# Kernel optimization log

Hardware: AMD Instinct MI355X
Metric: run time of the kernel (lower is better)

Reference implementation:

```python
import jax, jax.numpy as jnp
import numpy as np

N_NODES = 50000
N_EDGES = 800000
NEG_SLOPE = 0.2  # DGL GATConv leaky_relu default


def setup_inputs() -> dict:
    key = jax.random.key(0)
    ks = jax.random.split(key, 10)
    in_feats, n_hidden, n_classes = 256, 64, 47
    h1 = 4  # heads layer 1
    x = jax.random.normal(ks[0], (N_NODES, in_feats), dtype=jnp.float32)
    W1 = jax.random.normal(ks[1], (in_feats, h1 * n_hidden), dtype=jnp.float32) / np.sqrt(in_feats)
    al1 = jax.random.normal(ks[2], (h1, n_hidden), dtype=jnp.float32) * 0.1
    ar1 = jax.random.normal(ks[3], (h1, n_hidden), dtype=jnp.float32) * 0.1
    b1 = jnp.zeros((h1 * n_hidden,), dtype=jnp.float32)
    W2 = jax.random.normal(ks[4], (h1 * n_hidden, n_classes), dtype=jnp.float32) / np.sqrt(h1 * n_hidden)
    al2 = jax.random.normal(ks[5], (1, n_classes), dtype=jnp.float32) * 0.1
    ar2 = jax.random.normal(ks[6], (1, n_classes), dtype=jnp.float32) * 0.1
    b2 = jnp.zeros((n_classes,), dtype=jnp.float32)
    src = jax.random.randint(ks[7], (N_EDGES,), 0, N_NODES, dtype=jnp.int32)
    dst = jnp.sort(jax.random.randint(ks[8], (N_EDGES,), 0, N_NODES, dtype=jnp.int32))
    return {"x": x, "W1": W1, "al1": al1, "ar1": ar1, "b1": b1,
            "W2": W2, "al2": al2, "ar2": ar2, "b2": b2,
            "src": src, "dst": dst}


def gat_conv(h, W, al, ar, b, src, dst, heads, out_dim):
    # Linear projection -> [N, H, D]
    fs = (h @ W).reshape(-1, heads, out_dim)
    # Per-node attention logits: el/er [N, H]
    el = jnp.einsum('nhd,hd->nh', fs, al)
    er = jnp.einsum('nhd,hd->nh', fs, ar)
    # Edge-level attention: e [E, H]
    e = el[src] + er[dst]
    e = jnp.where(e > 0, e, NEG_SLOPE * e)  # leaky_relu
    # Segment softmax over incoming edges of each dst node
    m = jax.lax.stop_gradient(jax.ops.segment_max(e, dst, num_segments=N_NODES))
    ex = jnp.exp(e - m[dst])
    denom = jax.ops.segment_sum(ex, dst, num_segments=N_NODES)
    alpha = ex / denom[dst]  # [E, H]
    # Weighted scatter-aggregate of source features
    msg = alpha[:, :, None] * fs[src]  # [E, H, D]
    out = jax.ops.segment_sum(msg, dst, num_segments=N_NODES)  # [N, H, D]
    return out + b.reshape(1, heads, out_dim)


def reference(x, W1, al1, ar1, b1, W2, al2, ar2, b2, src, dst):
    # Layer 1: GATConv(256 -> 64, 4 heads) + relu activation, flatten heads
    h = gat_conv(x, W1, al1, ar1, b1, src, dst, heads=4, out_dim=64)
    h = jax.nn.relu(h).reshape(N_NODES, -1)  # [N, 256]
    # Layer 2: GATConv(256 -> 47, 1 head), no activation, mean over heads
    h = gat_conv(h, W2, al2, ar2, b2, src, dst, heads=1, out_dim=47)
    return h.mean(axis=1)  # [N, 47]
```

## Files before the change

### kernel.cpp

```cpp
#include <hip/hip_runtime.h>
#include <math.h>

#define NNODES 50000
#define NEDGES 800000
#define NEG_SLOPE 0.2f
#define MPAD 50048
#define CAPW 64

typedef __attribute__((ext_vector_type(8))) short short8;
typedef __attribute__((ext_vector_type(4))) float floatx4;

__device__ __forceinline__ unsigned short f2bf(float f) {
    union { float f; unsigned int u; } v; v.f = f;
    unsigned int r = v.u + 0x7FFFu + ((v.u >> 16) & 1u);
    return (unsigned short)(r >> 16);
}
__device__ __forceinline__ float bf2f(unsigned int s) {
    union { unsigned int u; float f; } v; v.u = s << 16; return v.f;
}
__device__ __forceinline__ float lrelu(float e) { return e > 0.f ? e : NEG_SLOPE * e; }

__global__ __launch_bounds__(256) void prep(const float* __restrict__ x,
                                            const float* __restrict__ W1,
                                            const float* __restrict__ W2,
                                            const int* __restrict__ dst,
                                            unsigned short* __restrict__ xb,
                                            unsigned short* __restrict__ bfrag1,
                                            unsigned short* __restrict__ bfrag2,
                                            unsigned short* __restrict__ h1b,
                                            int* __restrict__ row_ptr) {
    int b = blockIdx.x;
    if (b < 12512) {
        long e = ((long)b * 256 + threadIdx.x) * 4;
        const long NE = (long)NNODES * 256;
        ushort4 o;
        o.x = (e + 0 < NE) ? f2bf(x[e + 0]) : 0;
        o.y = (e + 1 < NE) ? f2bf(x[e + 1]) : 0;
        o.z = (e + 2 < NE) ? f2bf(x[e + 2]) : 0;
        o.w = (e + 3 < NE) ? f2bf(x[e + 3]) : 0;
        *(ushort4*)(xb + e) = o;
    } else if (b < 12708) {
        int n = (b - 12512) * 256 + threadIdx.x;
        if (n > NNODES) return;
        int lo = 0, hi = NEDGES;
        while (lo < hi) {
            int mid = (lo + hi) >> 1;
            if (dst[mid] < n) lo = mid + 1; else hi = mid;
        }
        row_ptr[n] = lo;
    } else if (b < 12740) {
        int c = (b - 12708) * 256 + threadIdx.x;
        int l = c & 63, kk = (c >> 6) & 7, t = c >> 9;
        int n = t * 16 + (l & 15);
        int kbase = kk * 32 + (l >> 4) * 8;
#pragma unroll
        for (int j = 0; j < 8; j++)
            bfrag1[c * 8 + j] = f2bf(W1[(kbase + j) * 256 + n]);
    } else if (b < 12746) {
        int c = (b - 12740) * 256 + threadIdx.x;
        int l = c & 63, kk = (c >> 6) & 7, t = c >> 9;
        int n = t * 16 + (l & 15);
        int kbase = kk * 32 + (l >> 4) * 8;
#pragma unroll
        for (int j = 0; j < 8; j++)
            bfrag2[c * 8 + j] = (n < 47) ? f2bf(W2[(kbase + j) * 47 + n]) : 0;
    } else {
        int row = NNODES + (b - 12746);
        h1b[(size_t)row * 256 + threadIdx.x] = 0;
    }
}

__global__ __launch_bounds__(256) void mfma_gemm1(const unsigned short* __restrict__ xb,
                                                  const unsigned short* __restrict__ bfrag,
                                                  const float* __restrict__ al1,
                                                  const float* __restrict__ ar1,
                                                  unsigned short* __restrict__ fs1b,
                                                  float* __restrict__ el,
                                                  float* __restrict__ er) {
    const int w = threadIdx.x >> 6;
    const int l = threadIdx.x & 63;
    const int bm = blockIdx.x * 128;
    const int head = blockIdx.y;
    const int n0 = head * 64;
    const int lm = l & 15, lk = l >> 4;

    floatx4 acc[2][4];
#pragma unroll
    for (int i = 0; i < 2; i++)
#pragma unroll
        for (int j = 0; j < 4; j++) acc[i][j] = (floatx4){0.f, 0.f, 0.f, 0.f};

    const int t0 = n0 >> 4;
#pragma unroll
    for (int kk = 0; kk < 8; kk++) {
        const unsigned short* abase = xb + (size_t)(bm + w * 32 + lm) * 256 + kk * 32 + lk * 8;
        short8 a0 = *(const short8*)(abase);
        short8 a1 = *(const short8*)(abase + 16 * 256);
        const unsigned short* bbase = bfrag + ((t0 * 8 + kk) * 64 + l) * 8;
        short8 b[4];
#pragma unroll
        for (int j = 0; j < 4; j++) b[j] = *(const short8*)(bbase + j * 8 * 64 * 8);
#pragma unroll
        for (int j = 0; j < 4; j++) {
            acc[0][j] = __builtin_amdgcn_mfma_f32_16x16x32_bf16(a0, b[j], acc[0][j], 0, 0, 0);
            acc[1][j] = __builtin_amdgcn_mfma_f32_16x16x32_bf16(a1, b[j], acc[1][j], 0, 0, 0);
        }
    }
#pragma unroll
    for (int i = 0; i < 2; i++) {
        int row0 = bm + w * 32 + i * 16 + lk * 4;
#pragma unroll
        for (int r = 0; r < 4; r++) {
            int row = row0 + r;
            if (row >= NNODES) continue;
#pragma unroll
            for (int j = 0; j < 4; j++) {
                int col = n0 + j * 16 + lm;
                fs1b[(size_t)row * 256 + col] = f2bf(acc[i][j][r]);
            }
        }
    }
    float alv[4], arv[4];
#pragma unroll
    for (int j = 0; j < 4; j++) {
        alv[j] = al1[head * 64 + j * 16 + lm];
        arv[j] = ar1[head * 64 + j * 16 + lm];
    }
#pragma unroll
    for (int i = 0; i < 2; i++) {
#pragma unroll
        for (int r = 0; r < 4; r++) {
            float pe = 0.f, pr = 0.f;
#pragma unroll
            for (int j = 0; j < 4; j++) {
                float fr = bf2f(f2bf(acc[i][j][r]));
                pe += fr * alv[j];
                pr += fr * arv[j];
            }
#pragma unroll
            for (int off = 1; off < 16; off <<= 1) {
                pe += __shfl_xor(pe, off);
                pr += __shfl_xor(pr, off);
            }
            int row = bm + w * 32 + i * 16 + lk * 4 + r;
            if (lm == 0 && row < NNODES) {
                el[row * 4 + head] = pe;
                er[row * 4 + head] = pr;
            }
        }
    }
}

__global__ __launch_bounds__(256) void mfma_gemm2(const unsigned short* __restrict__ h1b,
                                                  const unsigned short* __restrict__ bfrag,
                                                  const float* __restrict__ al2,
                                                  const float* __restrict__ ar2,
                                                  unsigned short* __restrict__ fs2b,
                                                  float* __restrict__ el,
                                                  float* __restrict__ er) {
    const int w = threadIdx.x >> 6;
    const int l = threadIdx.x & 63;
    const int bm = blockIdx.x * 128;
    const int lm = l & 15, lk = l >> 4;

    floatx4 acc[2][3];
#pragma unroll
    for (int i = 0; i < 2; i++)
#pragma unroll
        for (int j = 0; j < 3; j++) acc[i][j] = (floatx4){0.f, 0.f, 0.f, 0.f};

#pragma unroll
    for (int kk = 0; kk < 8; kk++) {
        const unsigned short* abase = h1b + (size_t)(bm + w * 32 + lm) * 256 + kk * 32 + lk * 8;
        short8 a0 = *(const short8*)(abase);
        short8 a1 = *(const short8*)(abase + 16 * 256);
        const unsigned short* bbase = bfrag + (size_t)(kk * 64 + l) * 8;
        short8 b[3];
#pragma unroll
        for (int j = 0; j < 3; j++) b[j] = *(const short8*)(bbase + j * (8 * 64 * 8));
#pragma unroll
        for (int j = 0; j < 3; j++) {
            acc[0][j] = __builtin_amdgcn_mfma_f32_16x16x32_bf16(a0, b[j], acc[0][j], 0, 0, 0);
            acc[1][j] = __builtin_amdgcn_mfma_f32_16x16x32_bf16(a1, b[j], acc[1][j], 0, 0, 0);
        }
    }
#pragma unroll
    for (int i = 0; i < 2; i++) {
        int row0 = bm + w * 32 + i * 16 + lk * 4;
#pragma unroll
        for (int r = 0; r < 4; r++) {
            int row = row0 + r;
            if (row >= NNODES) continue;
#pragma unroll
            for (int j = 0; j < 3; j++) {
                int col = j * 16 + lm;
                fs2b[(size_t)row * 48 + col] = f2bf(acc[i][j][r]);
            }
        }
    }
    float alv[3], arv[3];
#pragma unroll
    for (int j = 0; j < 3; j++) {
        int col = j * 16 + lm;
        alv[j] = (col < 47) ? al2[col] : 0.f;
        arv[j] = (col < 47) ? ar2[col] : 0.f;
    }
#pragma unroll
    for (int i = 0; i < 2; i++) {
#pragma unroll
        for (int r = 0; r < 4; r++) {
            float pe = 0.f, pr = 0.f;
#pragma unroll
            for (int j = 0; j < 3; j++) {
                float fr = bf2f(f2bf(acc[i][j][r]));
                pe += fr * alv[j];
                pr += fr * arv[j];
            }
#pragma unroll
            for (int off = 1; off < 16; off <<= 1) {
                pe += __shfl_xor(pe, off);
                pr += __shfl_xor(pr, off);
            }
            int row = bm + w * 32 + i * 16 + lk * 4 + r;
            if (lm == 0 && row < NNODES) {
                el[row] = pe;
                er[row] = pr;
            }
        }
    }
}

#define EDGE_ACC(G0, G1, W)                                              \
    a[0]  += (W) * bf2f((G0).x & 0xFFFFu); a[1]  += (W) * bf2f((G0).x >> 16); \
    a[2]  += (W) * bf2f((G0).y & 0xFFFFu); a[3]  += (W) * bf2f((G0).y >> 16); \
    a[4]  += (W) * bf2f((G0).z & 0xFFFFu); a[5]  += (W) * bf2f((G0).z >> 16); \
    a[6]  += (W) * bf2f((G0).w & 0xFFFFu); a[7]  += (W) * bf2f((G0).w >> 16); \
    a[8]  += (W) * bf2f((G1).x & 0xFFFFu); a[9]  += (W) * bf2f((G1).x >> 16); \
    a[10] += (W) * bf2f((G1).y & 0xFFFFu); a[11] += (W) * bf2f((G1).y >> 16); \
    a[12] += (W) * bf2f((G1).z & 0xFFFFu); a[13] += (W) * bf2f((G1).z >> 16); \
    a[14] += (W) * bf2f((G1).w & 0xFFFFu); a[15] += (W) * bf2f((G1).w >> 16);

__global__ __launch_bounds__(256) void agg1(const int* __restrict__ row_ptr,
                                            const int* __restrict__ src,
                                            const float* __restrict__ el,
                                            const float* __restrict__ er,
                                            const unsigned short* __restrict__ fs1b,
                                            const float* __restrict__ b1,
                                            unsigned short* __restrict__ h1b) {
    __shared__ float wcache[4][CAPW * 4];
    __shared__ int   scache[4][CAPW];
    const int q = threadIdx.x >> 6;
    const int l = threadIdx.x & 63;
    const int n = blockIdx.x * 4 + q;
    const int start = row_ptr[n], end = row_ptr[n + 1];
    const int deg = end - start;

    const float4 erv = *(const float4*)(er + n * 4);
    const int g = l >> 4;
    const int c16 = l & 15;
    const int hl = c16 >> 2;
    float a[16] = {};

    if (deg <= CAPW) {
        const bool act = l < deg;
        int sv = 0;
        float e0 = -1e30f, e1 = -1e30f, e2 = -1e30f, e3 = -1e30f;
        if (act) {
            sv = src[start + l];
            float4 e4 = *(const float4*)(el + sv * 4);
            e0 = lrelu(e4.x + erv.x);
            e1 = lrelu(e4.y + erv.y);
            e2 = lrelu(e4.z + erv.z);
            e3 = lrelu(e4.w + erv.w);
        }
        float M0 = e0, M1 = e1, M2 = e2, M3 = e3;
#pragma unroll
        for (int off = 32; off > 0; off >>= 1) {
            M0 = fmaxf(M0, __shfl_xor(M0, off));
            M1 = fmaxf(M1, __shfl_xor(M1, off));
            M2 = fmaxf(M2, __shfl_xor(M2, off));
            M3 = fmaxf(M3, __shfl_xor(M3, off));
        }
        float w0 = act ? __expf(e0 - M0) : 0.f;
        float w1 = act ? __expf(e1 - M1) : 0.f;
        float w2 = act ? __expf(e2 - M2) : 0.f;
        float w3 = act ? __expf(e3 - M3) : 0.f;
        float S0 = w0, S1 = w1, S2 = w2, S3 = w3;
#pragma unroll
        for (int off = 32; off > 0; off >>= 1) {
            S0 += __shfl_xor(S0, off);
            S1 += __shfl_xor(S1, off);
            S2 += __shfl_xor(S2, off);
            S3 += __shfl_xor(S3, off);
        }
        const float rs0 = deg > 0 ? 1.f / S0 : 0.f;
        const float rs1 = deg > 0 ? 1.f / S1 : 0.f;
        const float rs2 = deg > 0 ? 1.f / S2 : 0.f;
        const float rs3 = deg > 0 ? 1.f / S3 : 0.f;
        if (act) {
            scache[q][l] = sv;
            *(float4*)(&wcache[q][l * 4]) =
                make_float4(w0 * rs0, w1 * rs1, w2 * rs2, w3 * rs3);
        }
        int j = g;
        for (; j + 12 < deg; j += 16) {
            int s0 = scache[q][j],      s1 = scache[q][j + 4];
            int s2 = scache[q][j + 8],  s3 = scache[q][j + 12];
            float w0v = wcache[q][j * 4 + hl];
            float w1v = wcache[q][(j + 4) * 4 + hl];
            float w2v = wcache[q][(j + 8) * 4 + hl];
            float w3v = wcache[q][(j + 12) * 4 + hl];
            const unsigned short* p0 = fs1b + (size_t)s0 * 256 + c16 * 16;
            const unsigned short* p1 = fs1b + (size_t)s1 * 256 + c16 * 16;
            const unsigned short* p2 = fs1b + (size_t)s2 * 256 + c16 * 16;
            const unsigned short* p3 = fs1b + (size_t)s3 * 256 + c16 * 16;
            uint4 A0 = *(const uint4*)(p0), A1 = *(const uint4*)(p0 + 8);
            uint4 B0 = *(const uint4*)(p1), B1 = *(const uint4*)(p1 + 8);
            uint4 C0 = *(const uint4*)(p2), C1 = *(const uint4*)(p2 + 8);
            uint4 D0 = *(const uint4*)(p3), D1 = *(const uint4*)(p3 + 8);
            EDGE_ACC(A0, A1, w0v)
            EDGE_ACC(B0, B1, w1v)
            EDGE_ACC(C0, C1, w2v)
            EDGE_ACC(D0, D1, w3v)
        }
        for (; j + 4 < deg; j += 8) {
            int s0 = scache[q][j], s1 = scache[q][j + 4];
            float w0v = wcache[q][j * 4 + hl];
            float w1v = wcache[q][(j + 4) * 4 + hl];
            const unsigned short* p0 = fs1b + (size_t)s0 * 256 + c16 * 16;
            const unsigned short* p1 = fs1b + (size_t)s1 * 256 + c16 * 16;
            uint4 A0 = *(const uint4*)(p0), A1 = *(const uint4*)(p0 + 8);
            uint4 B0 = *(const uint4*)(p1), B1 = *(const uint4*)(p1 + 8);
            EDGE_ACC(A0, A1, w0v)
            EDGE_ACC(B0, B1, w1v)
        }
        if (j < deg) {
            int s0 = scache[q][j];
            float w0v = wcache[q][j * 4 + hl];
            const unsigned short* p0 = fs1b + (size_t)s0 * 256 + c16 * 16;
            uint4 A0 = *(const uint4*)(p0), A1 = *(const uint4*)(p0 + 8);
            EDGE_ACC(A0, A1, w0v)
        }
    } else {
        float m0 = -1e30f, m1 = -1e30f, m2 = -1e30f, m3 = -1e30f;
        float s0 = 0.f, s1 = 0.f, s2 = 0.f, s3 = 0.f;
        for (int i = start + l; i < end; i += 64) {
            float4 e4 = *(const float4*)(el + src[i] * 4);
            float e;
            e = lrelu(e4.x + erv.x); { float nm = fmaxf(m0, e); s0 = s0 * __expf(m0 - nm) + __expf(e - nm); m0 = nm; }
            e = lrelu(e4.y + erv.y); { float nm = fmaxf(m1, e); s1 = s1 * __expf(m1 - nm) + __expf(e - nm); m1 = nm; }
            e = lrelu(e4.z + erv.z); { float nm = fmaxf(m2, e); s2 = s2 * __expf(m2 - nm) + __expf(e - nm); m2 = nm; }
            e = lrelu(e4.w + erv.w); { float nm = fmaxf(m3, e); s3 = s3 * __expf(m3 - nm) + __expf(e - nm); m3 = nm; }
        }
        for (int off = 32; off > 0; off >>= 1) {
            float mo, so, nm;
            mo = __shfl_xor(m0, off); so = __shfl_xor(s0, off);
            nm = fmaxf(m0, mo); s0 = s0 * __expf(m0 - nm) + so * __expf(mo - nm); m0 = nm;
            mo = __shfl_xor(m1, off); so = __shfl_xor(s1, off);
            nm = fmaxf(m1, mo); s1 = s1 * __expf(m1 - nm) + so * __expf(mo - nm); m1 = nm;
            mo = __shfl_xor(m2, off); so = __shfl_xor(s2, off);
            nm = fmaxf(m2, mo); s2 = s2 * __expf(m2 - nm) + so * __expf(mo - nm); m2 = nm;
            mo = __shfl_xor(m3, off); so = __shfl_xor(s3, off);
            nm = fmaxf(m3, mo); s3 = s3 * __expf(m3 - nm) + so * __expf(mo - nm); m3 = nm;
        }
        const float Mh  = hl == 0 ? m0 : hl == 1 ? m1 : hl == 2 ? m2 : m3;
        const float Sh  = hl == 0 ? s0 : hl == 1 ? s1 : hl == 2 ? s2 : s3;
        const float rsh = deg > 0 ? 1.f / Sh : 0.f;
        const float ervh = hl == 0 ? erv.x : hl == 1 ? erv.y : hl == 2 ? erv.z : erv.w;
        for (int j = g; j < deg; j += 4) {
            int svj = src[start + j];
            float e = lrelu(el[svj * 4 + hl] + ervh);
            float wv = __expf(e - Mh) * rsh;
            const unsigned short* p = fs1b + (size_t)svj * 256 + c16 * 16;
            uint4 g0 = *(const uint4*)(p);
            uint4 g1 = *(const uint4*)(p + 8);
            EDGE_ACC(g0, g1, wv)
        }
    }
#pragma unroll
    for (int k = 0; k < 16; k++) {
        a[k] += __shfl_xor(a[k], 16);
        a[k] += __shfl_xor(a[k], 32);
    }
    if (g == 0) {
        const float* bb = b1 + c16 * 16;
        float4 b0 = *(const float4*)(bb);
        float4 b1v = *(const float4*)(bb + 4);
        float4 b2v = *(const float4*)(bb + 8);
        float4 b3v = *(const float4*)(bb + 12);
        float v[16];
        v[0]  = fmaxf(a[0]  + b0.x, 0.f); v[1]  = fmaxf(a[1]  + b0.y, 0.f);
        v[2]  = fmaxf(a[2]  + b0.z, 0.f); v[3]  = fmaxf(a[3]  + b0.w, 0.f);
        v[4]  = fmaxf(a[4]  + b1v.x, 0.f); v[5]  = fmaxf(a[5]  + b1v.y, 0.f);
        v[6]  = fmaxf(a[6]  + b1v.z, 0.f); v[7]  = fmaxf(a[7]  + b1v.w, 0.f);
        v[8]  = fmaxf(a[8]  + b2v.x, 0.f); v[9]  = fmaxf(a[9]  + b2v.y, 0.f);
        v[10] = fmaxf(a[10] + b2v.z, 0.f); v[11] = fmaxf(a[11] + b2v.w, 0.f);
        v[12] = fmaxf(a[12] + b3v.x, 0.f); v[13] = fmaxf(a[13] + b3v.y, 0.f);
        v[14] = fmaxf(a[14] + b3v.z, 0.f); v[15] = fmaxf(a[15] + b3v.w, 0.f);
        uint4 o0, o1;
        o0.x = (unsigned)f2bf(v[0])  | ((unsigned)f2bf(v[1])  << 16);
        o0.y = (unsigned)f2bf(v[2])  | ((unsigned)f2bf(v[3])  << 16);
        o0.z = (unsigned)f2bf(v[4])  | ((unsigned)f2bf(v[5])  << 16);
        o0.w = (unsigned)f2bf(v[6])  | ((unsigned)f2bf(v[7])  << 16);
        o1.x = (unsigned)f2bf(v[8])  | ((unsigned)f2bf(v[9])  << 16);
        o1.y = (unsigned)f2bf(v[10]) | ((unsigned)f2bf(v[11]) << 16);
        o1.z = (unsigned)f2bf(v[12]) | ((unsigned)f2bf(v[13]) << 16);
        o1.w = (unsigned)f2bf(v[14]) | ((unsigned)f2bf(v[15]) << 16);
        unsigned short* dstp = h1b + (size_t)n * 256 + c16 * 16;
        *(uint4*)(dstp) = o0;
        *(uint4*)(dstp + 8) = o1;
    }
}

__global__ __launch_bounds__(256) void agg2(const int* __restrict__ row_ptr,
                                            const int* __restrict__ src,
                                            const float* __restrict__ el,
                                            const float* __restrict__ er,
                                            const unsigned short* __restrict__ fs2b,
                                            const float* __restrict__ b2,
                                            float* __restrict__ out) {
    __shared__ float wcache[4][CAPW];
    __shared__ int   scache[4][CAPW];
    const int q = threadIdx.x >> 6;
    const int l = threadIdx.x & 63;
    const int n = blockIdx.x * 4 + q;
    const int start = row_ptr[n], end = row_ptr[n + 1];
    const int deg = end - start;
    const float erv = er[n];

    const int g4 = l >> 2;
    const int c4 = l & 3;
    float a[12] = {};

    if (deg <= CAPW) {
        const bool act = l < deg;
        int sv = 0;
        float e = -1e30f;
        if (act) {
            sv = src[start + l];
            e = lrelu(el[sv] + erv);
        }
        float M = e;
#pragma unroll
        for (int off = 32; off > 0; off >>= 1) M = fmaxf(M, __shfl_xor(M, off));
        float w = act ? __expf(e - M) : 0.f;
        float S = w;
#pragma unroll
        for (int off = 32; off > 0; off >>= 1) S += __shfl_xor(S, off);
        const float rs = deg > 0 ? 1.f / S : 0.f;
        if (act) {
            scache[q][l] = sv;
            wcache[q][l] = w * rs;
        }
        for (int j = g4; j < deg; j += 16) {
            int svj = scache[q][j];
            float wv = wcache[q][j];
            const unsigned short* p = fs2b + (size_t)svj * 48 + c4 * 12;
            uint2 u0 = *(const uint2*)(p);
            uint2 u1 = *(const uint2*)(p + 4);
            uint2 u2 = *(const uint2*)(p + 8);
            a[0]  += wv * bf2f(u0.x & 0xFFFFu); a[1]  += wv * bf2f(u0.x >> 16);
            a[2]  += wv * bf2f(u0.y & 0xFFFFu); a[3]  += wv * bf2f(u0.y >> 16);
            a[4]  += wv * bf2f(u1.x & 0xFFFFu); a[5]  += wv * bf2f(u1.x >> 16);
            a[6]  += wv * bf2f(u1.y & 0xFFFFu); a[7]  += wv * bf2f(u1.y >> 16);
            a[8]  += wv * bf2f(u2.x & 0xFFFFu); a[9]  += wv * bf2f(u2.x >> 16);
            a[10] += wv * bf2f(u2.y & 0xFFFFu); a[11] += wv * bf2f(u2.y >> 16);
        }
    } else {
        float m = -1e30f, s = 0.f;
        for (int i = start + l; i < end; i += 64) {
            float e = lrelu(el[src[i]] + erv);
            float nm = fmaxf(m, e);
            s = s * __expf(m - nm) + __expf(e - nm);
            m = nm;
        }
        for (int off = 32; off > 0; off >>= 1) {
            float mo = __shfl_xor(m, off), so = __shfl_xor(s, off);
            float nm = fmaxf(m, mo);
            s = s * __expf(m - nm) + so * __expf(mo - nm);
            m = nm;
        }
        const float rs = deg > 0 ? 1.f / s : 0.f;
        for (int j = g4; j < deg; j += 16) {
            int svj = src[start + j];
            float wv = __expf(lrelu(el[svj] + erv) - m) * rs;
            const unsigned short* p = fs2b + (size_t)svj * 48 + c4 * 12;
            uint2 u0 = *(const uint2*)(p);
            uint2 u1 = *(const uint2*)(p + 4);
            uint2 u2 = *(const uint2*)(p + 8);
            a[0]  += wv * bf2f(u0.x & 0xFFFFu); a[1]  += wv * bf2f(u0.x >> 16);
            a[2]  += wv * bf2f(u0.y & 0xFFFFu); a[3]  += wv * bf2f(u0.y >> 16);
            a[4]  += wv * bf2f(u1.x & 0xFFFFu); a[5]  += wv * bf2f(u1.x >> 16);
            a[6]  += wv * bf2f(u1.y & 0xFFFFu); a[7]  += wv * bf2f(u1.y >> 16);
            a[8]  += wv * bf2f(u2.x & 0xFFFFu); a[9]  += wv * bf2f(u2.x >> 16);
            a[10] += wv * bf2f(u2.y & 0xFFFFu); a[11] += wv * bf2f(u2.y >> 16);
        }
    }
#pragma unroll
    for (int k = 0; k < 12; k++) {
        a[k] += __shfl_xor(a[k], 4);
        a[k] += __shfl_xor(a[k], 8);
        a[k] += __shfl_xor(a[k], 16);
        a[k] += __shfl_xor(a[k], 32);
    }
    if (g4 == 0) {
        int ch0 = c4 * 12;
#pragma unroll
        for (int t = 0; t < 12; t++) {
            int ch = ch0 + t;
            if (ch < 47) out[(size_t)n * 47 + ch] = a[t] + b2[ch];
        }
    }
}

extern "C" void kernel_launch(void* const* d_in, const int* in_sizes, int n_in,
                              void* d_out, int out_size, void* d_ws, size_t ws_size,
                              hipStream_t stream) {
    const float* x   = (const float*)d_in[0];
    const float* W1  = (const float*)d_in[1];
    const float* al1 = (const float*)d_in[2];
    const float* ar1 = (const float*)d_in[3];
    const float* b1  = (const float*)d_in[4];
    const float* W2  = (const float*)d_in[5];
    const float* al2 = (const float*)d_in[6];
    const float* ar2 = (const float*)d_in[7];
    const float* b2  = (const float*)d_in[8];
    const int*   src = (const int*)d_in[9];
    const int*   dst = (const int*)d_in[10];
    float* out = (float*)d_out;

    char* ws = (char*)d_ws;
    size_t off = 0;
    auto alloc = [&](size_t bytes) {
        void* p = ws + off;
        off += (bytes + 255) & ~(size_t)255;
        return p;
    };
    int*            row_ptr = (int*)alloc((NNODES + 1) * sizeof(int));
    unsigned short* xb      = (unsigned short*)alloc((size_t)MPAD * 256 * 2);
    unsigned short* bfrag1  = (unsigned short*)alloc(16 * 8 * 64 * 8 * 2);
    unsigned short* bfrag2  = (unsigned short*)alloc(3 * 8 * 64 * 8 * 2);
    unsigned short* fs1b    = (unsigned short*)alloc((size_t)NNODES * 256 * 2);
    unsigned short* h1b     = (unsigned short*)alloc((size_t)MPAD * 256 * 2);
    unsigned short* fs2b    = (unsigned short*)alloc((size_t)NNODES * 48 * 2);
    float*          el1     = (float*)alloc((size_t)NNODES * 4 * sizeof(float));
    float*          er1     = (float*)alloc((size_t)NNODES * 4 * sizeof(float));
    float*          el2     = (float*)alloc((size_t)NNODES * sizeof(float));
    float*          er2     = (float*)alloc((size_t)NNODES * sizeof(float));
    (void)ws_size; (void)n_in; (void)in_sizes; (void)out_size;

    prep<<<12794, 256, 0, stream>>>(x, W1, W2, dst, xb, bfrag1, bfrag2, h1b, row_ptr);

    mfma_gemm1<<<dim3(MPAD / 128, 4), 256, 0, stream>>>(xb, bfrag1, al1, ar1, fs1b, el1, er1);
    agg1<<<NNODES / 4, 256, 0, stream>>>(row_ptr, src, el1, er1, fs1b, b1, h1b);

    mfma_gemm2<<<MPAD / 128, 256, 0, stream>>>(h1b, bfrag2, al2, ar2, fs2b, el2, er2);
    agg2<<<NNODES / 4, 256, 0, stream>>>(row_ptr, src, el2, er2, fs2b, b2, out);
}
```

Before: 271.4 us.

## Compute all four heads per GEMM1 block and simplify agg1 gather loop

GEMM1 now has each block compute all 256 output columns, i.e. all four heads, with 32 accumulator tiles per wave. The grid drops its head dimension, so the A tiles of x are read once instead of four times. This raises accumulator register use a lot, which may cut occupancy or cause spills. Separately, the agg1 edge loop loses its 4x/2x manual unroll and becomes a plain strided loop, which removes code size but also reduces memory-level parallelism for the feature gathers.

```diff
diff --git a/kernel.cpp b/kernel.cpp
--- a/kernel.cpp
+++ b/kernel.cpp
@@ -80,30 +80,25 @@
     const int w = threadIdx.x >> 6;
     const int l = threadIdx.x & 63;
     const int bm = blockIdx.x * 128;
-    const int head = blockIdx.y;
-    const int n0 = head * 64;
     const int lm = l & 15, lk = l >> 4;
 
-    floatx4 acc[2][4];
+    floatx4 acc[2][16];
 #pragma unroll
     for (int i = 0; i < 2; i++)
 #pragma unroll
-        for (int j = 0; j < 4; j++) acc[i][j] = (floatx4){0.f, 0.f, 0.f, 0.f};
-
-    const int t0 = n0 >> 4;
+        for (int t = 0; t < 16; t++) acc[i][t] = (floatx4){0.f, 0.f, 0.f, 0.f};
+
 #pragma unroll
     for (int kk = 0; kk < 8; kk++) {
         const unsigned short* abase = xb + (size_t)(bm + w * 32 + lm) * 256 + kk * 32 + lk * 8;
         short8 a0 = *(const short8*)(abase);
         short8 a1 = *(const short8*)(abase + 16 * 256);
-        const unsigned short* bbase = bfrag + ((t0 * 8 + kk) * 64 + l) * 8;
-        short8 b[4];
-#pragma unroll
-        for (int j = 0; j < 4; j++) b[j] = *(const short8*)(bbase + j * 8 * 64 * 8);
-#pragma unroll
-        for (int j = 0; j < 4; j++) {
-            acc[0][j] = __builtin_amdgcn_mfma_f32_16x16x32_bf16(a0, b[j], acc[0][j], 0, 0, 0);
-            acc[1][j] = __builtin_amdgcn_mfma_f32_16x16x32_bf16(a1, b[j], acc[1][j], 0, 0, 0);
+        const unsigned short* bbase = bfrag + (size_t)(kk * 64 + l) * 8;
+#pragma unroll
+        for (int t = 0; t < 16; t++) {
+            short8 b = *(const short8*)(bbase + (size_t)t * (8 * 64 * 8));
+            acc[0][t] = __builtin_amdgcn_mfma_f32_16x16x32_bf16(a0, b, acc[0][t], 0, 0, 0);
+            acc[1][t] = __builtin_amdgcn_mfma_f32_16x16x32_bf16(a1, b, acc[1][t], 0, 0, 0);
         }
     }
 #pragma unroll
@@ -114,38 +109,41 @@
             int row = row0 + r;
             if (row >= NNODES) continue;
 #pragma unroll
-            for (int j = 0; j < 4; j++) {
-                int col = n0 + j * 16 + lm;
-                fs1b[(size_t)row * 256 + col] = f2bf(acc[i][j][r]);
+            for (int t = 0; t < 16; t++) {
+                int col = t * 16 + lm;
+                fs1b[(size_t)row * 256 + col] = f2bf(acc[i][t][r]);
             }
         }
     }
-    float alv[4], arv[4];
-#pragma unroll
-    for (int j = 0; j < 4; j++) {
-        alv[j] = al1[head * 64 + j * 16 + lm];
-        arv[j] = ar1[head * 64 + j * 16 + lm];
-    }
-#pragma unroll
-    for (int i = 0; i < 2; i++) {
-#pragma unroll
-        for (int r = 0; r < 4; r++) {
-            float pe = 0.f, pr = 0.f;
-#pragma unroll
-            for (int j = 0; j < 4; j++) {
-                float fr = bf2f(f2bf(acc[i][j][r]));
-                pe += fr * alv[j];
-                pr += fr * arv[j];
-            }
-#pragma unroll
-            for (int off = 1; off < 16; off <<= 1) {
-                pe += __shfl_xor(pe, off);
-                pr += __shfl_xor(pr, off);
-            }
-            int row = bm + w * 32 + i * 16 + lk * 4 + r;
-            if (lm == 0 && row < NNODES) {
-                el[row * 4 + head] = pe;
-                er[row * 4 + head] = pr;
+#pragma unroll
+    for (int h = 0; h < 4; h++) {
+        float alv[4], arv[4];
+#pragma unroll
+        for (int j = 0; j < 4; j++) {
+            alv[j] = al1[h * 64 + j * 16 + lm];
+            arv[j] = ar1[h * 64 + j * 16 + lm];
+        }
+#pragma unroll
+        for (int i = 0; i < 2; i++) {
+#pragma unroll
+            for (int r = 0; r < 4; r++) {
+                float pe = 0.f, pr = 0.f;
+#pragma unroll
+                for (int j = 0; j < 4; j++) {
+                    float fr = bf2f(f2bf(acc[i][h * 4 + j][r]));
+                    pe += fr * alv[j];
+                    pr += fr * arv[j];
+                }
+#pragma unroll
+                for (int off = 1; off < 16; off <<= 1) {
+                    pe += __shfl_xor(pe, off);
+                    pr += __shfl_xor(pr, off);
+                }
+                int row = bm + w * 32 + i * 16 + lk * 4 + r;
+                if (lm == 0 && row < NNODES) {
+                    el[row * 4 + h] = pe;
+                    er[row * 4 + h] = pr;
+                }
             }
         }
     }
@@ -302,44 +300,13 @@
             *(float4*)(&wcache[q][l * 4]) =
                 make_float4(w0 * rs0, w1 * rs1, w2 * rs2, w3 * rs3);
         }
-        int j = g;
-        for (; j + 12 < deg; j += 16) {
-            int s0 = scache[q][j],      s1 = scache[q][j + 4];
-            int s2 = scache[q][j + 8],  s3 = scache[q][j + 12];
-            float w0v = wcache[q][j * 4 + hl];
-            float w1v = wcache[q][(j + 4) * 4 + hl];
-            float w2v = wcache[q][(j + 8) * 4 + hl];
-            float w3v = wcache[q][(j + 12) * 4 + hl];
-            const unsigned short* p0 = fs1b + (size_t)s0 * 256 + c16 * 16;
-            const unsigned short* p1 = fs1b + (size_t)s1 * 256 + c16 * 16;
-            const unsigned short* p2 = fs1b + (size_t)s2 * 256 + c16 * 16;
-            const unsigned short* p3 = fs1b + (size_t)s3 * 256 + c16 * 16;
-            uint4 A0 = *(const uint4*)(p0), A1 = *(const uint4*)(p0 + 8);
-            uint4 B0 = *(const uint4*)(p1), B1 = *(const uint4*)(p1 + 8);
-            uint4 C0 = *(const uint4*)(p2), C1 = *(const uint4*)(p2 + 8);
-            uint4 D0 = *(const uint4*)(p3), D1 = *(const uint4*)(p3 + 8);
-            EDGE_ACC(A0, A1, w0v)
-            EDGE_ACC(B0, B1, w1v)
-            EDGE_ACC(C0, C1, w2v)
-            EDGE_ACC(D0, D1, w3v)
-        }
-        for (; j + 4 < deg; j += 8) {
-            int s0 = scache[q][j], s1 = scache[q][j + 4];
-            float w0v = wcache[q][j * 4 + hl];
-            float w1v = wcache[q][(j + 4) * 4 + hl];
-            const unsigned short* p0 = fs1b + (size_t)s0 * 256 + c16 * 16;
-            const unsigned short* p1 = fs1b + (size_t)s1 * 256 + c16 * 16;
-            uint4 A0 = *(const uint4*)(p0), A1 = *(const uint4*)(p0 + 8);
-            uint4 B0 = *(const uint4*)(p1), B1 = *(const uint4*)(p1 + 8);
-            EDGE_ACC(A0, A1, w0v)
-            EDGE_ACC(B0, B1, w1v)
-        }
-        if (j < deg) {
-            int s0 = scache[q][j];
-            float w0v = wcache[q][j * 4 + hl];
-            const unsigned short* p0 = fs1b + (size_t)s0 * 256 + c16 * 16;
-            uint4 A0 = *(const uint4*)(p0), A1 = *(const uint4*)(p0 + 8);
-            EDGE_ACC(A0, A1, w0v)
+        for (int j = g; j < deg; j += 4) {
+            int svj = scache[q][j];
+            float wv = wcache[q][j * 4 + hl];
+            const unsigned short* p = fs1b + (size_t)svj * 256 + c16 * 16;
+            uint4 g0 = *(const uint4*)(p);
+            uint4 g1 = *(const uint4*)(p + 8);
+            EDGE_ACC(g0, g1, wv)
         }
     } else {
         float m0 = -1e30f, m1 = -1e30f, m2 = -1e30f, m3 = -1e30f;
@@ -551,7 +518,7 @@
 
     prep<<<12794, 256, 0, stream>>>(x, W1, W2, dst, xb, bfrag1, bfrag2, h1b, row_ptr);
 
-    mfma_gemm1<<<dim3(MPAD / 128, 4), 256, 0, stream>>>(xb, bfrag1, al1, ar1, fs1b, el1, er1);
+    mfma_gemm1<<<MPAD / 128, 256, 0, stream>>>(xb, bfrag1, al1, ar1, fs1b, el1, er1);
     agg1<<<NNODES / 4, 256, 0, stream>>>(row_ptr, src, el1, er1, fs1b, b1, h1b);
 
     mfma_gemm2<<<MPAD / 128, 256, 0, stream>>>(h1b, bfrag2, al2, ar2, fs2b, el2, er2);
```

New measurement: 287.8 us. 6.1% more time.
